# Kernel optimization log

Measured on AMD Instinct MI355X. Metric: run time of the kernel, lower is better.

Reference implementation:

```python
import jax, jax.numpy as jnp
import numpy as np


def setup_inputs() -> dict:
    key = jax.random.key(0)
    image = jax.random.uniform(key, (16, 3, 1024, 1024), dtype=jnp.float32)
    return {"image": image, "patch_size": 5}


def reference(image, patch_size):
    # Local (population) variance over a patch_size x patch_size sliding window
    # with reflect padding. Var = E[X^2] - E[X]^2, identical math to the
    # unfold-based mean((x - mean)^2) in the torch source.
    pad = patch_size // 2
    xp = jnp.pad(image, ((0, 0), (0, 0), (pad, pad), (pad, pad)), mode="reflect")
    n = jnp.asarray(patch_size * patch_size, dtype=image.dtype)

    def box_mean(x):
        # windowed sum via reduce_window, VALID -> output back to [B,C,H,W]
        s = jax.lax.reduce_window(
            x, jnp.asarray(0.0, x.dtype), jax.lax.add,
            window_dimensions=(1, 1, patch_size, patch_size),
            window_strides=(1, 1, 1, 1), padding="VALID")
        return s / n

    m = box_mean(xp)
    m2 = box_mean(xp * xp)
    return m2 - m * m
```

## Files before the change

kernel.cpp:

```cpp
#include <hip/hip_runtime.h>


constexpr int NT = 256;

__global__ __launch_bounds__(NT, 4)
void lvar5x5_reg_kernel(const float* __restrict__ in, float* __restrict__ out,
                        int H, int W) {
    const int tx = threadIdx.x & 63;
    const int ty = threadIdx.x >> 6;
    const int c0 = blockIdx.x * 256 + tx * 4;
    const int r0 = blockIdx.y * 32 + ty * 8;
    const size_t plane = (size_t)H * W;
    const float* __restrict__ img = in + (size_t)blockIdx.z * plane;
    float* __restrict__ o = out + (size_t)blockIdx.z * plane;

    const bool cL = (c0 == 0);
    const bool cR = (c0 == W - 4);
    const int a0 = cL ? 0 : c0 - 4;
    const int a2 = cR ? c0 : c0 + 4;

    float rh[5][4];
    float rq[5][4];
    float sh0 = 0.f, sh1 = 0.f, sh2 = 0.f, sh3 = 0.f;
    float sq0 = 0.f, sq1 = 0.f, sq2 = 0.f, sq3 = 0.f;

    const float inv = 1.0f / 25.0f;

#pragma unroll
    for (int i = 0; i < 12; ++i) {
        int gy = r0 - 2 + i;
        gy = (gy < 0) ? -gy : ((gy >= H) ? (2 * H - 2 - gy) : gy);
        const float* __restrict__ row = img + (size_t)gy * W;

        const float4 v0 = *reinterpret_cast<const float4*>(row + a0);
        const float4 v1 = *reinterpret_cast<const float4*>(row + c0);
        const float4 v2 = *reinterpret_cast<const float4*>(row + a2);

        const float x2 = v0.z;
        float       x3 = v0.w;
        const float x4 = v1.x, x5 = v1.y, x6 = v1.z, x7 = v1.w;
        float       x8 = v2.x;
        const float x9 = v2.y;
        if (cL) x3 = x5;
        if (cR) x8 = x6;

        const float h0 = x2 + x3 + x4 + x5 + x6;
        const float h1 = h0 - x2 + x7;
        const float h2 = h1 - x3 + x8;
        const float h3 = h2 - x4 + x9;

        const float y2 = x2 * x2, y3 = x3 * x3, y4 = x4 * x4, y5 = x5 * x5;
        const float y6 = x6 * x6, y7 = x7 * x7, y8 = x8 * x8, y9 = x9 * x9;
        const float q0 = y2 + y3 + y4 + y5 + y6;
        const float q1 = q0 - y2 + y7;
        const float q2 = q1 - y3 + y8;
        const float q3 = q2 - y4 + y9;

        const int s = i % 5;
        if (i >= 5) {
            sh0 -= rh[s][0]; sh1 -= rh[s][1]; sh2 -= rh[s][2]; sh3 -= rh[s][3];
            sq0 -= rq[s][0]; sq1 -= rq[s][1]; sq2 -= rq[s][2]; sq3 -= rq[s][3];
        }
        rh[s][0] = h0; rh[s][1] = h1; rh[s][2] = h2; rh[s][3] = h3;
        rq[s][0] = q0; rq[s][1] = q1; rq[s][2] = q2; rq[s][3] = q3;
        sh0 += h0; sh1 += h1; sh2 += h2; sh3 += h3;
        sq0 += q0; sq1 += q1; sq2 += q2; sq3 += q3;

        if (i >= 4) {
            float4 res;
            float m;
            m = sh0 * inv; res.x = fmaf(-m, m, sq0 * inv);
            m = sh1 * inv; res.y = fmaf(-m, m, sq1 * inv);
            m = sh2 * inv; res.z = fmaf(-m, m, sq2 * inv);
            m = sh3 * inv; res.w = fmaf(-m, m, sq3 * inv);
            *reinterpret_cast<float4*>(
                o + (size_t)(r0 + i - 4) * W + c0) = res;
        }
    }
}

extern "C" void kernel_launch(void* const* d_in, const int* in_sizes, int n_in,
                              void* d_out, int out_size, void* d_ws, size_t ws_size,
                              hipStream_t stream) {
    const float* image = (const float*)d_in[0];
    float* out = (float*)d_out;

    const int H = 1024, W = 1024;
    const int BC = out_size / (H * W);

    dim3 grid(W / 256, H / 32, BC);
    dim3 block(NT);
    lvar5x5_reg_kernel<<<grid, block, 0, stream>>>(image, out, H, W);
}
```

Before: 335.1 us.

## Compute vertical sums first and share horizontal neighbors through LDS

Reorders the separable box filter so each thread keeps a vertical running sum over its own column quad, loading one float4 per row instead of three. Horizontal neighbors are exchanged through double-buffered shared memory with a block barrier per output row. Each block now covers a full 1024-wide row strip of 32 rows, which cuts redundant neighbor loads and halo overhead. In exchange it adds a __syncthreads every row and raises LDS traffic.

```diff
diff --git a/kernel.cpp b/kernel.cpp
--- a/kernel.cpp
+++ b/kernel.cpp
@@ -2,80 +2,99 @@
 
 
 constexpr int NT = 256;
+constexpr int RH = 32;
 
 __global__ __launch_bounds__(NT, 4)
-void lvar5x5_reg_kernel(const float* __restrict__ in, float* __restrict__ out,
+void lvar5x5_sep_kernel(const float* __restrict__ in, float* __restrict__ out,
                         int H, int W) {
-    const int tx = threadIdx.x & 63;
-    const int ty = threadIdx.x >> 6;
-    const int c0 = blockIdx.x * 256 + tx * 4;
-    const int r0 = blockIdx.y * 32 + ty * 8;
+    const int tx = threadIdx.x;
+    const int c0 = tx * 4;
+    const int r0 = blockIdx.x * RH;
     const size_t plane = (size_t)H * W;
-    const float* __restrict__ img = in + (size_t)blockIdx.z * plane;
-    float* __restrict__ o = out + (size_t)blockIdx.z * plane;
+    const float* __restrict__ img = in + (size_t)blockIdx.y * plane;
+    float* __restrict__ o = out + (size_t)blockIdx.y * plane;
+
+    __shared__ float lsv[2][1024];
+    __shared__ float lsq[2][1024];
 
     const bool cL = (c0 == 0);
     const bool cR = (c0 == W - 4);
     const int a0 = cL ? 0 : c0 - 4;
     const int a2 = cR ? c0 : c0 + 4;
 
-    float rh[5][4];
-    float rq[5][4];
-    float sh0 = 0.f, sh1 = 0.f, sh2 = 0.f, sh3 = 0.f;
+    float ring[5][4];
+    float sv0 = 0.f, sv1 = 0.f, sv2 = 0.f, sv3 = 0.f;
     float sq0 = 0.f, sq1 = 0.f, sq2 = 0.f, sq3 = 0.f;
-
     const float inv = 1.0f / 25.0f;
 
-#pragma unroll
-    for (int i = 0; i < 12; ++i) {
+    auto row_ptr = [&](int i) -> const float4* {
         int gy = r0 - 2 + i;
         gy = (gy < 0) ? -gy : ((gy >= H) ? (2 * H - 2 - gy) : gy);
-        const float* __restrict__ row = img + (size_t)gy * W;
+        return reinterpret_cast<const float4*>(img + (size_t)gy * W + c0);
+    };
 
-        const float4 v0 = *reinterpret_cast<const float4*>(row + a0);
-        const float4 v1 = *reinterpret_cast<const float4*>(row + c0);
-        const float4 v2 = *reinterpret_cast<const float4*>(row + a2);
+    float4 vc = *row_ptr(0);
 
-        const float x2 = v0.z;
-        float       x3 = v0.w;
-        const float x4 = v1.x, x5 = v1.y, x6 = v1.z, x7 = v1.w;
-        float       x8 = v2.x;
-        const float x9 = v2.y;
-        if (cL) x3 = x5;
-        if (cR) x8 = x6;
-
-        const float h0 = x2 + x3 + x4 + x5 + x6;
-        const float h1 = h0 - x2 + x7;
-        const float h2 = h1 - x3 + x8;
-        const float h3 = h2 - x4 + x9;
-
-        const float y2 = x2 * x2, y3 = x3 * x3, y4 = x4 * x4, y5 = x5 * x5;
-        const float y6 = x6 * x6, y7 = x7 * x7, y8 = x8 * x8, y9 = x9 * x9;
-        const float q0 = y2 + y3 + y4 + y5 + y6;
-        const float q1 = q0 - y2 + y7;
-        const float q2 = q1 - y3 + y8;
-        const float q3 = q2 - y4 + y9;
+#pragma unroll
+    for (int i = 0; i < RH + 4; ++i) {
+        float4 vn;
+        if (i < RH + 3) vn = *row_ptr(i + 1);
 
         const int s = i % 5;
         if (i >= 5) {
-            sh0 -= rh[s][0]; sh1 -= rh[s][1]; sh2 -= rh[s][2]; sh3 -= rh[s][3];
-            sq0 -= rq[s][0]; sq1 -= rq[s][1]; sq2 -= rq[s][2]; sq3 -= rq[s][3];
+            const float o0 = ring[s][0], o1 = ring[s][1],
+                        o2 = ring[s][2], o3 = ring[s][3];
+            sv0 -= o0; sv1 -= o1; sv2 -= o2; sv3 -= o3;
+            sq0 = fmaf(-o0, o0, sq0); sq1 = fmaf(-o1, o1, sq1);
+            sq2 = fmaf(-o2, o2, sq2); sq3 = fmaf(-o3, o3, sq3);
         }
-        rh[s][0] = h0; rh[s][1] = h1; rh[s][2] = h2; rh[s][3] = h3;
-        rq[s][0] = q0; rq[s][1] = q1; rq[s][2] = q2; rq[s][3] = q3;
-        sh0 += h0; sh1 += h1; sh2 += h2; sh3 += h3;
-        sq0 += q0; sq1 += q1; sq2 += q2; sq3 += q3;
+        ring[s][0] = vc.x; ring[s][1] = vc.y; ring[s][2] = vc.z; ring[s][3] = vc.w;
+        sv0 += vc.x; sv1 += vc.y; sv2 += vc.z; sv3 += vc.w;
+        sq0 = fmaf(vc.x, vc.x, sq0); sq1 = fmaf(vc.y, vc.y, sq1);
+        sq2 = fmaf(vc.z, vc.z, sq2); sq3 = fmaf(vc.w, vc.w, sq3);
 
         if (i >= 4) {
+            const int sl = i & 1;
+            *reinterpret_cast<float4*>(&lsv[sl][c0]) =
+                make_float4(sv0, sv1, sv2, sv3);
+            *reinterpret_cast<float4*>(&lsq[sl][c0]) =
+                make_float4(sq0, sq1, sq2, sq3);
+            __syncthreads();
+
+            const float4 u0 = *reinterpret_cast<const float4*>(&lsv[sl][a0]);
+            const float4 u2 = *reinterpret_cast<const float4*>(&lsv[sl][a2]);
+            const float4 w0 = *reinterpret_cast<const float4*>(&lsq[sl][a0]);
+            const float4 w2 = *reinterpret_cast<const float4*>(&lsq[sl][a2]);
+
+            const float t2 = u0.z;
+            float       t3 = cL ? sv1 : u0.w;
+            float       t8 = cR ? sv2 : u2.x;
+            const float t9 = u2.y;
+
+            const float g2 = w0.z;
+            float       g3 = cL ? sq1 : w0.w;
+            float       g8 = cR ? sq2 : w2.x;
+            const float g9 = w2.y;
+
+            const float h0 = t2 + t3 + sv0 + sv1 + sv2;
+            const float h1 = h0 - t2 + sv3;
+            const float h2 = h1 - t3 + t8;
+            const float h3 = h2 - sv0 + t9;
+
+            const float q0 = g2 + g3 + sq0 + sq1 + sq2;
+            const float q1 = q0 - g2 + sq3;
+            const float q2 = q1 - g3 + g8;
+            const float q3 = q2 - sq0 + g9;
+
             float4 res;
             float m;
-            m = sh0 * inv; res.x = fmaf(-m, m, sq0 * inv);
-            m = sh1 * inv; res.y = fmaf(-m, m, sq1 * inv);
-            m = sh2 * inv; res.z = fmaf(-m, m, sq2 * inv);
-            m = sh3 * inv; res.w = fmaf(-m, m, sq3 * inv);
-            *reinterpret_cast<float4*>(
-                o + (size_t)(r0 + i - 4) * W + c0) = res;
+            m = h0 * inv; res.x = fmaf(-m, m, q0 * inv);
+            m = h1 * inv; res.y = fmaf(-m, m, q1 * inv);
+            m = h2 * inv; res.z = fmaf(-m, m, q2 * inv);
+            m = h3 * inv; res.w = fmaf(-m, m, q3 * inv);
+            *reinterpret_cast<float4*>(o + (size_t)(r0 + i - 4) * W + c0) = res;
         }
+        vc = vn;
     }
 }
 
@@ -88,7 +107,7 @@
     const int H = 1024, W = 1024;
     const int BC = out_size / (H * W);
 
-    dim3 grid(W / 256, H / 32, BC);
+    dim3 grid(H / RH, BC);
     dim3 block(NT);
-    lvar5x5_reg_kernel<<<grid, block, 0, stream>>>(image, out, H, W);
+    lvar5x5_sep_kernel<<<grid, block, 0, stream>>>(image, out, H, W);
 }
```

After: 344.1 us. 1.03x slower.

## Process full-width 64-row strips per block with rotating 5-row register window

Applied to the files above, without the earlier changes.

Each block now covers a full 1024-wide row strip of 64 rows, with each thread walking down 64 rows instead of 8. The vertical window is kept as five rotating register structs and summed directly, replacing the running add/subtract sums. This cuts the halo re-read overhead from 12 loaded rows per 8 outputs to 68 per 64. The trade-off is a smaller grid (768 blocks) and a loop that is only partly unrolled, which may reduce parallelism and the number of loads in flight.

```diff
diff --git a/kernel.cpp b/kernel.cpp
--- a/kernel.cpp
+++ b/kernel.cpp
@@ -2,81 +2,89 @@
 
 
 constexpr int NT = 256;
+constexpr int RB = 64;
+
+struct Row8 { float h0, h1, h2, h3, q0, q1, q2, q3; };
 
 __global__ __launch_bounds__(NT, 4)
-void lvar5x5_reg_kernel(const float* __restrict__ in, float* __restrict__ out,
-                        int H, int W) {
-    const int tx = threadIdx.x & 63;
-    const int ty = threadIdx.x >> 6;
-    const int c0 = blockIdx.x * 256 + tx * 4;
-    const int r0 = blockIdx.y * 32 + ty * 8;
+void lvar5x5_rolled_kernel(const float* __restrict__ in, float* __restrict__ out,
+                           int H, int W) {
+    const int tx = threadIdx.x;
+    const int c0 = tx * 4;
+    const int r0 = blockIdx.x * RB;
     const size_t plane = (size_t)H * W;
-    const float* __restrict__ img = in + (size_t)blockIdx.z * plane;
-    float* __restrict__ o = out + (size_t)blockIdx.z * plane;
+    const float* __restrict__ img = in + (size_t)blockIdx.y * plane;
+    float* __restrict__ o = out + (size_t)blockIdx.y * plane;
 
-    const bool cL = (c0 == 0);
-    const bool cR = (c0 == W - 4);
+    const bool cL = (tx == 0);
+    const bool cR = (tx == NT - 1);
     const int a0 = cL ? 0 : c0 - 4;
     const int a2 = cR ? c0 : c0 + 4;
-
-    float rh[5][4];
-    float rq[5][4];
-    float sh0 = 0.f, sh1 = 0.f, sh2 = 0.f, sh3 = 0.f;
-    float sq0 = 0.f, sq1 = 0.f, sq2 = 0.f, sq3 = 0.f;
-
     const float inv = 1.0f / 25.0f;
 
-#pragma unroll
-    for (int i = 0; i < 12; ++i) {
-        int gy = r0 - 2 + i;
+    Row8 A, B, C, D, E;
+
+    auto ROW = [&](int ri, Row8& s) {
+        int gy = r0 - 2 + ri;
         gy = (gy < 0) ? -gy : ((gy >= H) ? (2 * H - 2 - gy) : gy);
         const float* __restrict__ row = img + (size_t)gy * W;
-
         const float4 v0 = *reinterpret_cast<const float4*>(row + a0);
         const float4 v1 = *reinterpret_cast<const float4*>(row + c0);
         const float4 v2 = *reinterpret_cast<const float4*>(row + a2);
 
         const float x2 = v0.z;
-        float       x3 = v0.w;
+        const float x3 = cL ? v1.y : v0.w;
         const float x4 = v1.x, x5 = v1.y, x6 = v1.z, x7 = v1.w;
-        float       x8 = v2.x;
+        const float x8 = cR ? v1.z : v2.x;
         const float x9 = v2.y;
-        if (cL) x3 = x5;
-        if (cR) x8 = x6;
 
-        const float h0 = x2 + x3 + x4 + x5 + x6;
-        const float h1 = h0 - x2 + x7;
-        const float h2 = h1 - x3 + x8;
-        const float h3 = h2 - x4 + x9;
+        s.h0 = x2 + x3 + x4 + x5 + x6;
+        s.h1 = s.h0 - x2 + x7;
+        s.h2 = s.h1 - x3 + x8;
+        s.h3 = s.h2 - x4 + x9;
 
         const float y2 = x2 * x2, y3 = x3 * x3, y4 = x4 * x4, y5 = x5 * x5;
         const float y6 = x6 * x6, y7 = x7 * x7, y8 = x8 * x8, y9 = x9 * x9;
-        const float q0 = y2 + y3 + y4 + y5 + y6;
-        const float q1 = q0 - y2 + y7;
-        const float q2 = q1 - y3 + y8;
-        const float q3 = q2 - y4 + y9;
+        s.q0 = y2 + y3 + y4 + y5 + y6;
+        s.q1 = s.q0 - y2 + y7;
+        s.q2 = s.q1 - y3 + y8;
+        s.q3 = s.q2 - y4 + y9;
+    };
 
-        const int s = i % 5;
-        if (i >= 5) {
-            sh0 -= rh[s][0]; sh1 -= rh[s][1]; sh2 -= rh[s][2]; sh3 -= rh[s][3];
-            sq0 -= rq[s][0]; sq1 -= rq[s][1]; sq2 -= rq[s][2]; sq3 -= rq[s][3];
-        }
-        rh[s][0] = h0; rh[s][1] = h1; rh[s][2] = h2; rh[s][3] = h3;
-        rq[s][0] = q0; rq[s][1] = q1; rq[s][2] = q2; rq[s][3] = q3;
-        sh0 += h0; sh1 += h1; sh2 += h2; sh3 += h3;
-        sq0 += q0; sq1 += q1; sq2 += q2; sq3 += q3;
+    auto EMIT = [&](int j, const Row8& a, const Row8& b, const Row8& c,
+                    const Row8& d, const Row8& e) {
+        float4 res;
+        float hs, qs, m;
+        hs = a.h0 + b.h0 + c.h0 + d.h0 + e.h0;
+        qs = a.q0 + b.q0 + c.q0 + d.q0 + e.q0;
+        m = hs * inv; res.x = fmaf(-m, m, qs * inv);
+        hs = a.h1 + b.h1 + c.h1 + d.h1 + e.h1;
+        qs = a.q1 + b.q1 + c.q1 + d.q1 + e.q1;
+        m = hs * inv; res.y = fmaf(-m, m, qs * inv);
+        hs = a.h2 + b.h2 + c.h2 + d.h2 + e.h2;
+        qs = a.q2 + b.q2 + c.q2 + d.q2 + e.q2;
+        m = hs * inv; res.z = fmaf(-m, m, qs * inv);
+        hs = a.h3 + b.h3 + c.h3 + d.h3 + e.h3;
+        qs = a.q3 + b.q3 + c.q3 + d.q3 + e.q3;
+        m = hs * inv; res.w = fmaf(-m, m, qs * inv);
+        *reinterpret_cast<float4*>(o + (size_t)(r0 + j) * W + c0) = res;
+    };
 
-        if (i >= 4) {
-            float4 res;
-            float m;
-            m = sh0 * inv; res.x = fmaf(-m, m, sq0 * inv);
-            m = sh1 * inv; res.y = fmaf(-m, m, sq1 * inv);
-            m = sh2 * inv; res.z = fmaf(-m, m, sq2 * inv);
-            m = sh3 * inv; res.w = fmaf(-m, m, sq3 * inv);
-            *reinterpret_cast<float4*>(
-                o + (size_t)(r0 + i - 4) * W + c0) = res;
-        }
+    ROW(0, A); ROW(1, B); ROW(2, C); ROW(3, D);
+
+#pragma unroll 1
+    for (int j = 0; j < RB - 4; j += 5) {
+        ROW(j + 4, E); EMIT(j + 0, A, B, C, D, E);
+        ROW(j + 5, A); EMIT(j + 1, B, C, D, E, A);
+        ROW(j + 6, B); EMIT(j + 2, C, D, E, A, B);
+        ROW(j + 7, C); EMIT(j + 3, D, E, A, B, C);
+        ROW(j + 8, D); EMIT(j + 4, E, A, B, C, D);
     }
+
+    ROW(64, E); EMIT(60, A, B, C, D, E);
+    ROW(65, A); EMIT(61, B, C, D, E, A);
+    ROW(66, B); EMIT(62, C, D, E, A, B);
+    ROW(67, C); EMIT(63, D, E, A, B, C);
 }
 
 extern "C" void kernel_launch(void* const* d_in, const int* in_sizes, int n_in,
@@ -88,7 +96,7 @@
     const int H = 1024, W = 1024;
     const int BC = out_size / (H * W);
 
-    dim3 grid(W / 256, H / 32, BC);
+    dim3 grid(H / RB, BC);
     dim3 block(NT);
-    lvar5x5_reg_kernel<<<grid, block, 0, stream>>>(image, out, H, W);
+    lvar5x5_rolled_kernel<<<grid, block, 0, stream>>>(image, out, H, W);
 }
```

Result: no change. 338.8 us (+1.1%).
